# Performance work log

Hardware: AMD Instinct MI355X
Metric: run time of the kernel (lower is better)

## Reference

```python
import jax, jax.numpy as jnp
import numpy as np

VAR0, VAR1 = 0.1, 0.2          # SSD variances
IOU_THRESH = 0.5
NUM_CLASSES = 21
NEGPOS_RATIO = 3
ALPHA = 1.0


def mid_to_corner(b):
    # [cx,cy,w,h] -> [xmin,ymin,xmax,ymax]
    return jnp.concatenate([b[:, :2] - b[:, 2:] / 2, b[:, :2] + b[:, 2:] / 2], axis=1)


def jaccard(box_a, box_b):
    # box_a [n,4], box_b [P,4] corner form -> IoU [n,P]
    lt = jnp.maximum(box_a[:, None, :2], box_b[None, :, :2])
    rb = jnp.minimum(box_a[:, None, 2:], box_b[None, :, 2:])
    wh = jnp.clip(rb - lt, 0.0)
    inter = wh[..., 0] * wh[..., 1]
    area_a = (box_a[:, 2] - box_a[:, 0]) * (box_a[:, 3] - box_a[:, 1])
    area_b = (box_b[:, 2] - box_b[:, 0]) * (box_b[:, 3] - box_b[:, 1])
    union = area_a[:, None] + area_b[None, :] - inter
    return inter / union


def encode_offset(matched, priors):
    # matched corner form [P,4], priors center form [P,4]
    g_cxcy = ((matched[:, :2] + matched[:, 2:]) / 2 - priors[:, :2]) / (VAR0 * priors[:, 2:])
    g_wh = jnp.log((matched[:, 2:] - matched[:, :2]) / priors[:, 2:]) / VAR1
    return jnp.concatenate([g_cxcy, g_wh], axis=1)


def match_one(gt_box, gt_cls, valid, priors_corner, priors_mid):
    # gt_box [n,4], gt_cls [n], valid [n] bool; priors [P,4]
    n = gt_box.shape[0]
    P = priors_corner.shape[0]
    ovl = jaccard(gt_box, priors_corner)                    # [n,P]
    ovl = jnp.where(valid[:, None], ovl, -1.0)              # mask padded GTs
    best_truth_idx = jnp.argmax(ovl, axis=0)                # [P]
    best_truth_ovl = jnp.max(ovl, axis=0)                   # [P]
    best_prior_idx = jnp.argmax(ovl, axis=1)                # [n]
    bpi = jnp.where(valid, best_prior_idx, P)               # OOB for padded -> dropped
    best_truth_ovl = best_truth_ovl.at[bpi].set(2.0, mode='drop')
    best_truth_idx = best_truth_idx.at[bpi].set(jnp.arange(n), mode='drop')
    matches = gt_box[best_truth_idx]                        # [P,4]
    loc = encode_offset(matches, priors_mid)                # [P,4]
    conf = gt_cls[best_truth_idx].astype(jnp.int32) + 1     # [P]
    conf = jnp.where(best_truth_ovl < IOU_THRESH, 0, conf)
    return loc, conf


def setup_inputs() -> dict:
    key = jax.random.key(0)
    k = jax.random.split(key, 8)
    B, P, C, NMAX = 64, 8732, 21, 50
    confidence = jax.random.normal(k[0], (B, P, C), dtype=jnp.float32)
    location = 0.1 * jax.random.normal(k[1], (B, P, 4), dtype=jnp.float32)
    cxcy = jax.random.uniform(k[2], (P, 2), minval=0.05, maxval=0.95)
    pwh = jax.random.uniform(k[3], (P, 2), minval=0.05, maxval=0.4)
    prior_boxes = jnp.concatenate([cxcy, pwh], axis=1).astype(jnp.float32)
    xymin = jax.random.uniform(k[4], (B, NMAX, 2), minval=0.0, maxval=0.6)
    gwh = jax.random.uniform(k[5], (B, NMAX, 2), minval=0.05, maxval=0.35)
    cls = jax.random.randint(k[6], (B, NMAX), 0, C - 1).astype(jnp.float32)
    labels = jnp.concatenate([xymin, xymin + gwh, cls[..., None]], axis=-1).astype(jnp.float32)
    obj_count = jax.random.randint(k[7], (B, 1), 1, NMAX + 1).astype(jnp.int32)
    return {"confidence": confidence, "location": location,
            "prior_boxes": prior_boxes, "labels": labels, "obj_count": obj_count}


def reference(confidence, location, prior_boxes, labels, obj_count):
    B, P, C = confidence.shape
    NMAX = labels.shape[1]
    priors_corner = mid_to_corner(prior_boxes)
    valid = jnp.arange(NMAX)[None, :] < obj_count            # [B,NMAX]
    loc_t, conf_t = jax.vmap(match_one, in_axes=(0, 0, 0, None, None))(
        labels[..., :4], labels[..., 4], valid, priors_corner, prior_boxes)
    # loc_t [B,P,4] float, conf_t [B,P] int32

    pos = conf_t > 0                                          # [B,P]
    # smooth-L1 over positive anchors (sum reduction)
    d = jnp.abs(location - loc_t)
    sl1 = jnp.where(d < 1.0, 0.5 * d * d, d - 0.5)
    loss_loc = jnp.sum(sl1 * pos[..., None].astype(sl1.dtype))

    # hard negative mining score: global-max logsumexp minus target logit
    bc = confidence.reshape(-1, C)
    x_max = jnp.max(bc)
    lse = jnp.log(jnp.sum(jnp.exp(bc - x_max), axis=1)) + x_max
    tgt_logit = jnp.take_along_axis(bc, conf_t.reshape(-1, 1), axis=1)[:, 0]
    loss_c = (lse - tgt_logit).reshape(B, P)
    loss_c = jnp.where(pos, 0.0, loss_c)
    loss_idx = jnp.argsort(-loss_c, axis=1)                   # descending sort
    idx_rank = jnp.argsort(loss_idx, axis=1)
    num_pos = jnp.sum(pos.astype(jnp.int32), axis=1, keepdims=True)   # [B,1]
    num_neg = jnp.clip(NEGPOS_RATIO * num_pos, None, P - 1)
    neg = idx_rank < num_neg                                  # [B,P]

    # standard cross entropy over selected (pos|neg) anchors, sum reduction
    logp = jax.nn.log_softmax(confidence, axis=-1)            # [B,P,C]
    nll = -jnp.take_along_axis(logp, conf_t[..., None], axis=-1)[..., 0]
    sel = jnp.logical_or(pos, neg)
    loss_conf = jnp.sum(nll * sel.astype(nll.dtype))

    N = jnp.sum(num_pos).astype(confidence.dtype)
    return (ALPHA * loss_loc / N, loss_conf / N)
```

## Files before the change

kernel.cpp:

```cpp
#include <hip/hip_runtime.h>
#include <math.h>

#define Bn 64
#define Pn 8732
#define Cn 21
#define NMAXn 50
#define PX 35

__global__ __launch_bounds__(256) void k_matchbp(const float* __restrict__ labels,
                                                 const int* __restrict__ objc,
                                                 const float* __restrict__ priors,
                                                 int* __restrict__ match,
                                                 int* __restrict__ bp) {
    const int bx = blockIdx.x;
    const int tid = threadIdx.x;
    __shared__ float lab[NMAXn * 5];
    __shared__ int cnt_s;
    __shared__ float sv[256];
    __shared__ int si[256];

    if (bx < Bn * PX) {
        const int b = bx / PX;
        const int p = (bx % PX) * 256 + tid;
        for (int i = tid; i < NMAXn * 5; i += 256) lab[i] = labels[b * NMAXn * 5 + i];
        if (tid == 0) cnt_s = objc[b];
        __syncthreads();
        if (p >= Pn) return;
        const float4 pr = reinterpret_cast<const float4*>(priors)[p];
        const float px0 = pr.x - 0.5f * pr.z, py0 = pr.y - 0.5f * pr.w;
        const float px1 = pr.x + 0.5f * pr.z, py1 = pr.y + 0.5f * pr.w;
        const float parea = (px1 - px0) * (py1 - py0);
        const int cnt = cnt_s;
        float best = -1.0f;
        int bidx = 0;
        for (int n = 0; n < cnt; ++n) {
            const float gx0 = lab[n * 5 + 0], gy0 = lab[n * 5 + 1];
            const float gx1 = lab[n * 5 + 2], gy1 = lab[n * 5 + 3];
            const float lx = fmaxf(gx0, px0), ly = fmaxf(gy0, py0);
            const float rx = fminf(gx1, px1), ry = fminf(gy1, py1);
            const float w = fmaxf(rx - lx, 0.0f), h = fmaxf(ry - ly, 0.0f);
            const float inter = w * h;
            const float ga = (gx1 - gx0) * (gy1 - gy0);
            const float v = inter / (ga + parea - inter);
            if (v > best) { best = v; bidx = n; }
        }
        match[(size_t)b * Pn + p] = (bidx << 1) | (best >= 0.5f ? 1 : 0);
    } else {
        const int idx = bx - Bn * PX;
        const int b = idx / NMAXn;
        const int n = idx % NMAXn;
        if (n >= objc[b]) return;
        const float gx0 = labels[(b * NMAXn + n) * 5 + 0];
        const float gy0 = labels[(b * NMAXn + n) * 5 + 1];
        const float gx1 = labels[(b * NMAXn + n) * 5 + 2];
        const float gy1 = labels[(b * NMAXn + n) * 5 + 3];
        const float ga = (gx1 - gx0) * (gy1 - gy0);
        float best = -1.0f;
        int bidx = 0;
        for (int p = tid; p < Pn; p += 256) {
            const float4 pr = reinterpret_cast<const float4*>(priors)[p];
            const float px0 = pr.x - 0.5f * pr.z, py0 = pr.y - 0.5f * pr.w;
            const float px1 = pr.x + 0.5f * pr.z, py1 = pr.y + 0.5f * pr.w;
            const float lx = fmaxf(gx0, px0), ly = fmaxf(gy0, py0);
            const float rx = fminf(gx1, px1), ry = fminf(gy1, py1);
            const float w = fmaxf(rx - lx, 0.0f), h = fmaxf(ry - ly, 0.0f);
            const float inter = w * h;
            const float pa = (px1 - px0) * (py1 - py0);
            const float v = inter / (ga + pa - inter);
            if (v > best) { best = v; bidx = p; }
        }
        sv[tid] = best;
        si[tid] = bidx;
        __syncthreads();
        for (int s = 128; s > 0; s >>= 1) {
            if (tid < s) {
                const float ov = sv[tid + s];
                const int oi = si[tid + s];
                if (ov > sv[tid] || (ov == sv[tid] && oi < si[tid])) {
                    sv[tid] = ov;
                    si[tid] = oi;
                }
            }
            __syncthreads();
        }
        if (tid == 0) bp[b * NMAXn + n] = si[0];
    }
}

__global__ __launch_bounds__(256) void k_force(const int* __restrict__ objc,
                                               const int* __restrict__ bp,
                                               int* __restrict__ match) {
    __shared__ int sbp[Bn * NMAXn];
    const int tid = threadIdx.x;
    for (int i = tid; i < Bn * NMAXn; i += 256) sbp[i] = bp[i];
    __syncthreads();
    if (tid < Bn) {
        const int cnt = objc[tid];
        const size_t base = (size_t)tid * Pn;
        for (int n = 0; n < cnt; ++n) match[base + sbp[tid * NMAXn + n]] = (n << 1) | 1;
    }
}

__global__ __launch_bounds__(256) void k_main(const float* __restrict__ conf,
                                              const float* __restrict__ loc,
                                              const float* __restrict__ priors,
                                              const float* __restrict__ labels,
                                              const int* __restrict__ match,
                                              float* __restrict__ lc,
                                              float* __restrict__ part_loc,
                                              float* __restrict__ part_nll,
                                              int* __restrict__ part_np) {
    const int b = blockIdx.y;
    const int px = blockIdx.x;
    const int p0 = px * 256;
    const int tid = threadIdx.x;
    const int rows = min(256, Pn - p0);
    const int p = p0 + ((tid < rows) ? tid : 0);
    const size_t gi = (size_t)b * Pn + p;
    const int w = match[gi];

    __shared__ float sconf[256 * Cn];
    __shared__ float lab[NMAXn * 5];
    const float4* src = reinterpret_cast<const float4*>(conf + ((size_t)b * Pn + p0) * Cn);
    const int n4 = rows * Cn / 4;
    for (int i = tid; i < n4; i += 256) reinterpret_cast<float4*>(sconf)[i] = src[i];
    for (int i = tid; i < NMAXn * 5; i += 256) lab[i] = labels[b * NMAXn * 5 + i];
    __syncthreads();

    float my_loc = 0.0f, my_nll = 0.0f;
    int my_np = 0;
    if (tid < rows) {
        const int ti = w >> 1;
        const int ct = (w & 1) ? ((int)lab[ti * 5 + 4] + 1) : 0;
        const float* row = sconf + tid * Cn;
        float m = row[0];
#pragma unroll
        for (int j = 1; j < Cn; ++j) m = fmaxf(m, row[j]);
        float s2 = 0.0f;
#pragma unroll
        for (int j = 0; j < Cn; ++j) s2 += __expf(row[j] - m);
        const float nll = __logf(s2) + m - row[ct];
        if (ct > 0) {
            lc[gi] = 0.0f;
            my_np = 1;
            my_nll = nll;
            const float4 pr = reinterpret_cast<const float4*>(priors)[p];
            const float gx0 = lab[ti * 5 + 0], gy0 = lab[ti * 5 + 1];
            const float gx1 = lab[ti * 5 + 2], gy1 = lab[ti * 5 + 3];
            const float tx = ((gx0 + gx1) * 0.5f - pr.x) / (0.1f * pr.z);
            const float ty = ((gy0 + gy1) * 0.5f - pr.y) / (0.1f * pr.w);
            const float tw = __logf((gx1 - gx0) / pr.z) * 5.0f;
            const float th = __logf((gy1 - gy0) / pr.w) * 5.0f;
            const float4 l = reinterpret_cast<const float4*>(loc)[gi];
            float d;
            d = fabsf(l.x - tx); my_loc += (d < 1.0f) ? 0.5f * d * d : d - 0.5f;
            d = fabsf(l.y - ty); my_loc += (d < 1.0f) ? 0.5f * d * d : d - 0.5f;
            d = fabsf(l.z - tw); my_loc += (d < 1.0f) ? 0.5f * d * d : d - 0.5f;
            d = fabsf(l.w - th); my_loc += (d < 1.0f) ? 0.5f * d * d : d - 0.5f;
        } else {
            lc[gi] = nll;
        }
    }
    for (int off = 32; off > 0; off >>= 1) {
        my_loc += __shfl_down(my_loc, off);
        my_nll += __shfl_down(my_nll, off);
        my_np += __shfl_down(my_np, off);
    }
    __shared__ float rl[4], rn[4];
    __shared__ int rp[4];
    const int wid = tid >> 6, lane = tid & 63;
    if (lane == 0) { rl[wid] = my_loc; rn[wid] = my_nll; rp[wid] = my_np; }
    __syncthreads();
    if (tid == 0) {
        const int g = b * PX + px;
        part_loc[g] = rl[0] + rl[1] + rl[2] + rl[3];
        part_nll[g] = rn[0] + rn[1] + rn[2] + rn[3];
        part_np[g] = rp[0] + rp[1] + rp[2] + rp[3];
    }
}

__global__ __launch_bounds__(512) void k_neg(const float* __restrict__ lc,
                                             const int* __restrict__ part_np,
                                             float* __restrict__ negsum) {
    const int b = blockIdx.x;
    const int tid = threadIdx.x;
    __shared__ float s[Pn];
    __shared__ int np_sh;
    __shared__ unsigned bounds[2];
    __shared__ int redc[8];
    __shared__ float redf[8];
    const float4* src = reinterpret_cast<const float4*>(lc + (size_t)b * Pn);
    for (int i = tid; i < Pn / 4; i += 512) reinterpret_cast<float4*>(s)[i] = src[i];
    int npl = (tid < PX) ? part_np[b * PX + tid] : 0;
    for (int off = 32; off > 0; off >>= 1) npl += __shfl_down(npl, off);
    if (tid == 0) { np_sh = npl; bounds[0] = 0u; bounds[1] = 0x7F800000u; }
    __syncthreads();
    const int k = min(3 * np_sh, Pn - 1);
    const int wid = tid >> 6, lane = tid & 63;
    while (true) {
        const unsigned lo = bounds[0], hi = bounds[1];
        if (hi - lo <= 1u) break;
        const unsigned mid = lo + ((hi - lo) >> 1);
        const float fm = __uint_as_float(mid);
        int c = 0;
        for (int i = tid; i < Pn / 4; i += 512) {
            const float4 v = reinterpret_cast<const float4*>(s)[i];
            c += (v.x >= fm) + (v.y >= fm) + (v.z >= fm) + (v.w >= fm);
        }
        for (int off = 32; off > 0; off >>= 1) c += __shfl_down(c, off);
        if (lane == 0) redc[wid] = c;
        __syncthreads();
        if (tid == 0) {
            int t = 0;
#pragma unroll
            for (int i = 0; i < 8; ++i) t += redc[i];
            if (t >= k) bounds[0] = mid;
            else bounds[1] = mid;
        }
        __syncthreads();
    }
    const float v = __uint_as_float(bounds[0]);
    float sm = 0.0f;
    int c = 0;
    for (int i = tid; i < Pn / 4; i += 512) {
        const float4 q = reinterpret_cast<const float4*>(s)[i];
        if (q.x > v) { sm += q.x; ++c; }
        if (q.y > v) { sm += q.y; ++c; }
        if (q.z > v) { sm += q.z; ++c; }
        if (q.w > v) { sm += q.w; ++c; }
    }
    for (int off = 32; off > 0; off >>= 1) {
        sm += __shfl_down(sm, off);
        c += __shfl_down(c, off);
    }
    if (lane == 0) { redf[wid] = sm; redc[wid] = c; }
    __syncthreads();
    if (tid == 0) {
        float st = 0.0f;
        int ct = 0;
#pragma unroll
        for (int i = 0; i < 8; ++i) { st += redf[i]; ct += redc[i]; }
        negsum[b] = st + (float)(k - ct) * v;
    }
}

__global__ __launch_bounds__(256) void k_final(const float* __restrict__ part_loc,
                                               const float* __restrict__ part_nll,
                                               const int* __restrict__ part_np,
                                               const float* __restrict__ negsum,
                                               float* __restrict__ out) {
    const int tid = threadIdx.x;
    float sl = 0.0f, sn = 0.0f;
    int np = 0;
    for (int i = tid; i < Bn * PX; i += 256) {
        sl += part_loc[i];
        sn += part_nll[i];
        np += part_np[i];
    }
    if (tid < Bn) sn += negsum[tid];
    for (int off = 32; off > 0; off >>= 1) {
        sl += __shfl_down(sl, off);
        sn += __shfl_down(sn, off);
        np += __shfl_down(np, off);
    }
    __shared__ float rl[4], rn[4];
    __shared__ int rp[4];
    const int wid = tid >> 6, lane = tid & 63;
    if (lane == 0) { rl[wid] = sl; rn[wid] = sn; rp[wid] = np; }
    __syncthreads();
    if (tid == 0) {
        const float fN = (float)(rp[0] + rp[1] + rp[2] + rp[3]);
        out[0] = (rl[0] + rl[1] + rl[2] + rl[3]) / fN;
        out[1] = (rn[0] + rn[1] + rn[2] + rn[3]) / fN;
    }
}

extern "C" void kernel_launch(void* const* d_in, const int* in_sizes, int n_in,
                              void* d_out, int out_size, void* d_ws, size_t ws_size,
                              hipStream_t stream) {
    const float* conf = (const float*)d_in[0];
    const float* loc = (const float*)d_in[1];
    const float* priors = (const float*)d_in[2];
    const float* labels = (const float*)d_in[3];
    const int* objc = (const int*)d_in[4];
    float* out = (float*)d_out;

    float* part_loc = (float*)d_ws;
    float* part_nll = part_loc + Bn * PX;
    int* part_np = (int*)(part_nll + Bn * PX);
    float* negsum = (float*)(part_np + Bn * PX);
    int* bp = (int*)(negsum + Bn);
    int* match = bp + Bn * NMAXn;
    float* lc = (float*)(match + (size_t)Bn * Pn);

    k_matchbp<<<Bn * PX + Bn * NMAXn, 256, 0, stream>>>(labels, objc, priors, match, bp);
    k_force<<<1, 256, 0, stream>>>(objc, bp, match);
    dim3 g(PX, Bn);
    k_main<<<g, 256, 0, stream>>>(conf, loc, priors, labels, match, lc,
                                  part_loc, part_nll, part_np);
    k_neg<<<Bn, 512, 0, stream>>>(lc, part_np, negsum);
    k_final<<<1, 256, 0, stream>>>(part_loc, part_nll, part_np, negsum, out);
}
```

Measured before the change: 81.21 us.

## Fold forced matching into main kernel and final reduction into neg kernel

Removes the single-block k_force kernel: each k_main block now scans the per-image best-prior list to apply forced matches itself. The final reduction kernel is also removed, and the last k_neg block to finish (found with an atomic counter) does the global sum. The bisection loop in k_neg runs a fixed 31 iterations, with per-iteration shared atomic slots so each step needs one barrier instead of two. This cuts two launches and a serial single-block kernel, in exchange for a 50-entry compare loop per prior and the threadfence/atomic handshake.

```diff
diff --git a/kernel.cpp b/kernel.cpp
--- a/kernel.cpp
+++ b/kernel.cpp
@@ -87,29 +87,18 @@
     }
 }
 
-__global__ __launch_bounds__(256) void k_force(const int* __restrict__ objc,
-                                               const int* __restrict__ bp,
-                                               int* __restrict__ match) {
-    __shared__ int sbp[Bn * NMAXn];
-    const int tid = threadIdx.x;
-    for (int i = tid; i < Bn * NMAXn; i += 256) sbp[i] = bp[i];
-    __syncthreads();
-    if (tid < Bn) {
-        const int cnt = objc[tid];
-        const size_t base = (size_t)tid * Pn;
-        for (int n = 0; n < cnt; ++n) match[base + sbp[tid * NMAXn + n]] = (n << 1) | 1;
-    }
-}
-
 __global__ __launch_bounds__(256) void k_main(const float* __restrict__ conf,
                                               const float* __restrict__ loc,
                                               const float* __restrict__ priors,
                                               const float* __restrict__ labels,
+                                              const int* __restrict__ objc,
                                               const int* __restrict__ match,
+                                              const int* __restrict__ bp,
                                               float* __restrict__ lc,
                                               float* __restrict__ part_loc,
                                               float* __restrict__ part_nll,
-                                              int* __restrict__ part_np) {
+                                              int* __restrict__ part_np,
+                                              int* __restrict__ done) {
     const int b = blockIdx.y;
     const int px = blockIdx.x;
     const int p0 = px * 256;
@@ -119,19 +108,28 @@
     const size_t gi = (size_t)b * Pn + p;
     const int w = match[gi];
 
+    if (b == 0 && px == 0 && tid == 0) *done = 0;
+
     __shared__ float sconf[256 * Cn];
     __shared__ float lab[NMAXn * 5];
+    __shared__ int sbp[NMAXn];
     const float4* src = reinterpret_cast<const float4*>(conf + ((size_t)b * Pn + p0) * Cn);
     const int n4 = rows * Cn / 4;
     for (int i = tid; i < n4; i += 256) reinterpret_cast<float4*>(sconf)[i] = src[i];
     for (int i = tid; i < NMAXn * 5; i += 256) lab[i] = labels[b * NMAXn * 5 + i];
+    if (tid < NMAXn) sbp[tid] = (tid < objc[b]) ? bp[b * NMAXn + tid] : -1;
     __syncthreads();
 
     float my_loc = 0.0f, my_nll = 0.0f;
     int my_np = 0;
     if (tid < rows) {
-        const int ti = w >> 1;
-        const int ct = (w & 1) ? ((int)lab[ti * 5 + 4] + 1) : 0;
+        int ti = w >> 1;
+        int fl = w & 1;
+#pragma unroll
+        for (int n = 0; n < NMAXn; ++n) {
+            if (sbp[n] == p) { ti = n; fl = 1; }
+        }
+        const int ct = fl ? ((int)lab[ti * 5 + 4] + 1) : 0;
         const float* row = sconf + tid * Cn;
         float m = row[0];
 #pragma unroll
@@ -180,26 +178,36 @@
 }
 
 __global__ __launch_bounds__(512) void k_neg(const float* __restrict__ lc,
+                                             const float* __restrict__ part_loc,
+                                             const float* __restrict__ part_nll,
                                              const int* __restrict__ part_np,
-                                             float* __restrict__ negsum) {
+                                             float* __restrict__ negsum,
+                                             int* __restrict__ done,
+                                             float* __restrict__ out) {
     const int b = blockIdx.x;
     const int tid = threadIdx.x;
     __shared__ float s[Pn];
+    __shared__ int cslot[32];
     __shared__ int np_sh;
-    __shared__ unsigned bounds[2];
+    __shared__ float redf[8], redf2[8];
     __shared__ int redc[8];
-    __shared__ float redf[8];
+    __shared__ int islast;
+
     const float4* src = reinterpret_cast<const float4*>(lc + (size_t)b * Pn);
     for (int i = tid; i < Pn / 4; i += 512) reinterpret_cast<float4*>(s)[i] = src[i];
-    int npl = (tid < PX) ? part_np[b * PX + tid] : 0;
-    for (int off = 32; off > 0; off >>= 1) npl += __shfl_down(npl, off);
-    if (tid == 0) { np_sh = npl; bounds[0] = 0u; bounds[1] = 0x7F800000u; }
+    if (tid < 32) cslot[tid] = 0;
+    if (tid < 64) {
+        int npl = (tid < PX) ? part_np[b * PX + tid] : 0;
+        for (int off = 32; off > 0; off >>= 1) npl += __shfl_down(npl, off);
+        if (tid == 0) np_sh = npl;
+    }
     __syncthreads();
     const int k = min(3 * np_sh, Pn - 1);
     const int wid = tid >> 6, lane = tid & 63;
-    while (true) {
-        const unsigned lo = bounds[0], hi = bounds[1];
-        if (hi - lo <= 1u) break;
+
+    unsigned lo = 0u, hi = 0x7F800000u;
+#pragma unroll 1
+    for (int it = 0; it < 31; ++it) {
         const unsigned mid = lo + ((hi - lo) >> 1);
         const float fm = __uint_as_float(mid);
         int c = 0;
@@ -208,18 +216,14 @@
             c += (v.x >= fm) + (v.y >= fm) + (v.z >= fm) + (v.w >= fm);
         }
         for (int off = 32; off > 0; off >>= 1) c += __shfl_down(c, off);
-        if (lane == 0) redc[wid] = c;
+        if (lane == 0) atomicAdd(&cslot[it], c);
         __syncthreads();
-        if (tid == 0) {
-            int t = 0;
-#pragma unroll
-            for (int i = 0; i < 8; ++i) t += redc[i];
-            if (t >= k) bounds[0] = mid;
-            else bounds[1] = mid;
-        }
-        __syncthreads();
-    }
-    const float v = __uint_as_float(bounds[0]);
+        const int tot = cslot[it];
+        if (tot >= k) lo = mid;
+        else hi = mid;
+    }
+    const float v = __uint_as_float(lo);
+
     float sm = 0.0f;
     int c = 0;
     for (int i = tid; i < Pn / 4; i += 512) {
@@ -241,18 +245,16 @@
 #pragma unroll
         for (int i = 0; i < 8; ++i) { st += redf[i]; ct += redc[i]; }
         negsum[b] = st + (float)(k - ct) * v;
-    }
-}
-
-__global__ __launch_bounds__(256) void k_final(const float* __restrict__ part_loc,
-                                               const float* __restrict__ part_nll,
-                                               const int* __restrict__ part_np,
-                                               const float* __restrict__ negsum,
-                                               float* __restrict__ out) {
-    const int tid = threadIdx.x;
+        __threadfence();
+        islast = (atomicAdd(done, 1) == Bn - 1) ? 1 : 0;
+    }
+    __syncthreads();
+    if (!islast) return;
+    __threadfence();
+
     float sl = 0.0f, sn = 0.0f;
     int np = 0;
-    for (int i = tid; i < Bn * PX; i += 256) {
+    for (int i = tid; i < Bn * PX; i += 512) {
         sl += part_loc[i];
         sn += part_nll[i];
         np += part_np[i];
@@ -263,15 +265,16 @@
         sn += __shfl_down(sn, off);
         np += __shfl_down(np, off);
     }
-    __shared__ float rl[4], rn[4];
-    __shared__ int rp[4];
-    const int wid = tid >> 6, lane = tid & 63;
-    if (lane == 0) { rl[wid] = sl; rn[wid] = sn; rp[wid] = np; }
+    if (lane == 0) { redf[wid] = sn; redf2[wid] = sl; redc[wid] = np; }
     __syncthreads();
     if (tid == 0) {
-        const float fN = (float)(rp[0] + rp[1] + rp[2] + rp[3]);
-        out[0] = (rl[0] + rl[1] + rl[2] + rl[3]) / fN;
-        out[1] = (rn[0] + rn[1] + rn[2] + rn[3]) / fN;
+        float tsl = 0.0f, tsn = 0.0f;
+        int tnp = 0;
+#pragma unroll
+        for (int i = 0; i < 8; ++i) { tsl += redf2[i]; tsn += redf[i]; tnp += redc[i]; }
+        const float fN = (float)tnp;
+        out[0] = tsl / fN;
+        out[1] = tsn / fN;
     }
 }
 
@@ -292,12 +295,11 @@
     int* bp = (int*)(negsum + Bn);
     int* match = bp + Bn * NMAXn;
     float* lc = (float*)(match + (size_t)Bn * Pn);
+    int* done = (int*)(lc + (size_t)Bn * Pn);
 
     k_matchbp<<<Bn * PX + Bn * NMAXn, 256, 0, stream>>>(labels, objc, priors, match, bp);
-    k_force<<<1, 256, 0, stream>>>(objc, bp, match);
     dim3 g(PX, Bn);
-    k_main<<<g, 256, 0, stream>>>(conf, loc, priors, labels, match, lc,
-                                  part_loc, part_nll, part_np);
-    k_neg<<<Bn, 512, 0, stream>>>(lc, part_np, negsum);
-    k_final<<<1, 256, 0, stream>>>(part_loc, part_nll, part_np, negsum, out);
+    k_main<<<g, 256, 0, stream>>>(conf, loc, priors, labels, objc, match, bp, lc,
+                                  part_loc, part_nll, part_np, done);
+    k_neg<<<Bn, 512, 0, stream>>>(lc, part_loc, part_nll, part_np, negsum, done, out);
 }
```

New measurement: 79.65 us. Within noise of the previous version (-1.9%).
